# Kernel tuning notes

Hardware: AMD Instinct MI355X
Metric: run time of the kernel (lower is better)

## Reference

```python
import jax, jax.numpy as jnp
import numpy as np

NUM_OBJS = 180   # len(vocab['node'])
NUM_PREDS = 180  # len(vocab['edge'])
D = 128          # embedding_dim == gconv_dim
H = 512          # gconv_hidden_dim
L = 5            # gconv_num_layers (1 GraphTripleConv + 4 in GraphTripleConvNet; identical shapes)
G = 64           # number of graphs in the batch
O = 5000         # total nodes
T = 20000        # total triples (edges)
SC = 0.02        # param init scale


def setup_inputs() -> dict:
    key = jax.random.key(0)
    ks = jax.random.split(key, 18)
    objs = jax.random.randint(ks[0], (O,), 0, NUM_OBJS + 1)
    s = jax.random.randint(ks[1], (T,), 0, O)
    o = jax.random.randint(ks[2], (T,), 0, O)
    p = jax.random.randint(ks[3], (T,), 0, NUM_PREDS)
    triples = jnp.stack([s, p, o], axis=1)
    obj_to_img = jnp.sort(jax.random.randint(ks[4], (O,), 0, G))
    f32 = jnp.float32
    return {
        'objs': objs,
        'triples': triples,
        'obj_to_img': obj_to_img,
        'obj_emb': jax.random.normal(ks[5], (NUM_OBJS + 1, D), f32) * SC,
        'pred_emb': jax.random.normal(ks[6], (NUM_PREDS, D), f32) * SC,
        # net1: [3D -> H -> 2H + D], stacked over L layers
        'n1w1': jax.random.normal(ks[7], (L, 3 * D, H), f32) * SC,
        'n1b1': jnp.zeros((L, H), f32),
        'n1w2': jax.random.normal(ks[8], (L, H, 2 * H + D), f32) * SC,
        'n1b2': jnp.zeros((L, 2 * H + D), f32),
        # net2: [H -> H -> D], stacked over L layers
        'n2w1': jax.random.normal(ks[9], (L, H, H), f32) * SC,
        'n2b1': jnp.zeros((L, H), f32),
        'n2w2': jax.random.normal(ks[10], (L, H, D), f32) * SC,
        'n2b2': jnp.zeros((L, D), f32),
        # AttentionModule: per-graph attention pooling over node vectors
        'att_w': jax.random.normal(ks[11], (D,), f32) * SC,
        'att_b': jnp.zeros((), f32),
    }


def _mlp2(x, w1, b1, w2, b2):
    # build_mlp with final_nonlinearity=True -> Linear,ReLU,Linear,ReLU
    return jax.nn.relu(jax.nn.relu(x @ w1 + b1) @ w2 + b2)


def _triple_conv(ov, pv, s, o, n1w1, n1b1, n1w2, n1b2, n2w1, n2b1, n2w2, n2b2):
    n_obj = ov.shape[0]
    t = jnp.concatenate([ov[s], pv, ov[o]], axis=1)          # [T, 3D]
    new_t = _mlp2(t, n1w1, n1b1, n1w2, n1b2)                 # [T, 2H+D]
    new_s = new_t[:, :H]
    new_p = new_t[:, H:H + D]
    new_o = new_t[:, H + D:]
    pooled = jnp.zeros((n_obj, H), new_t.dtype).at[s].add(new_s).at[o].add(new_o)
    counts = jnp.zeros((n_obj,), new_t.dtype).at[s].add(1.0).at[o].add(1.0)
    pooled = pooled / jnp.clip(counts, 1.0)[:, None]         # pooling='avg'
    new_ov = _mlp2(pooled, n2w1, n2b1, n2w2, n2b2)           # [O, D]
    return new_ov, new_p


def reference(objs, triples, obj_to_img, obj_emb, pred_emb,
              n1w1, n1b1, n1w2, n1b2, n2w1, n2b1, n2w2, n2b2, att_w, att_b):
    s, p, o = triples[:, 0], triples[:, 1], triples[:, 2]
    ov = obj_emb[objs]     # [O, D]
    pv = pred_emb[p]       # [T, D]
    for l in range(L):
        ov, pv = _triple_conv(ov, pv, s, o,
                              n1w1[l], n1b1[l], n1w2[l], n1b2[l],
                              n2w1[l], n2b1[l], n2w2[l], n2b2[l])
    # AttentionModule: segment softmax attention pooling per graph, broadcast back
    scores = ov @ att_w + att_b                               # [O]
    m = jax.ops.segment_max(scores, obj_to_img, num_segments=G)
    e = jnp.exp(scores - m[obj_to_img])
    z = jax.ops.segment_sum(e, obj_to_img, num_segments=G)
    w = e / z[obj_to_img]
    g = jax.ops.segment_sum(w[:, None] * ov, obj_to_img, num_segments=G)  # [G, D]
    graph_vecs = g[obj_to_img]                                # [O, D]
    return jnp.concatenate([ov, graph_vecs], axis=1)          # [O, 2D]
```

## Files before the change

kernel.cpp:

```cpp
#include <hip/hip_runtime.h>
#include <math.h>

#define O_N 5000
#define T_N 20000
#define D_ 128
#define H_ 512
#define L_ 5
#define G_ 64
#define NT_ 1152
#define NPRED 180

typedef unsigned short ushort_t;
typedef __attribute__((ext_vector_type(8))) __bf16 bf16x8;
typedef __attribute__((ext_vector_type(4))) float f32x4;

__device__ inline float bf2f(ushort_t u) {
    union { unsigned u32; float f; } cv; cv.u32 = ((unsigned)u) << 16; return cv.f;
}
__device__ inline ushort_t f2bf(float f) {
    union { float f; unsigned u; } cv; cv.f = f;
    unsigned x = cv.u;
    unsigned r = x + 0x7FFFu + ((x >> 16) & 1u);
    return (ushort_t)(r >> 16);
}

__device__ inline void gload16(const void* g, void* l) {
    __builtin_amdgcn_global_load_lds(
        (const __attribute__((address_space(1))) unsigned int*)g,
        (__attribute__((address_space(3))) unsigned int*)l,
        16, 0, 0);
}

template<int GATHER, int WRITE_F32>
__global__ __launch_bounds__(256)
void mfma_gemm(const ushort_t* __restrict__ A,
               const ushort_t* __restrict__ Bt,
               const float* __restrict__ bias,
               ushort_t* __restrict__ Cb,
               float* __restrict__ Cf,
               int M, int N, int K, int ldc, int ntiles,
               const int* __restrict__ triples,
               const ushort_t* __restrict__ ovb,
               const ushort_t* __restrict__ P, int pstride, int pmap)
{
    __shared__ __align__(16) ushort_t smem[16384];

    const int tid  = threadIdx.x;
    const int lane = tid & 63;
    const int wid  = tid >> 6;
    const int wm   = wid & 1;
    const int wn   = wid >> 1;

    const int nwg = gridDim.x;
    const int q = nwg >> 3, r = nwg & 7;
    const int xcd = blockIdx.x & 7, i8 = blockIdx.x >> 3;
    const int lid = (xcd < r ? xcd * (q + 1) : r * (q + 1) + (xcd - r) * q) + i8;
    const int bm = (lid / ntiles) * 128;
    const int bn = (lid % ntiles) * 128;

    const int u0 = wid * 64 + lane;
    const int u1 = u0 + 256;
    const int r0 = u0 >> 2;
    const int r1 = u1 >> 2;
    const int ks0 = (((u0 & 3) ^ ((r0 >> 1) & 3)) << 3);
    const int ks1 = (((u1 & 3) ^ ((r1 >> 1) & 3)) << 3);

    const int ga0 = min(bm + r0, M - 1);
    const int ga1 = min(bm + r1, M - 1);
    int s0 = 0, o0 = 0, p0 = 0, s1 = 0, o1 = 0, p1 = 0;
    if (GATHER) {
        s0 = triples[ga0 * 3];  p0 = pmap ? triples[ga0 * 3 + 1] : ga0;  o0 = triples[ga0 * 3 + 2];
        s1 = triples[ga1 * 3];  p1 = pmap ? triples[ga1 * 3 + 1] : ga1;  o1 = triples[ga1 * 3 + 2];
    }
    const int gb0 = bn + r0;
    const int gb1 = bn + r1;

    int offA[4], offB[4];
    #pragma unroll
    for (int i = 0; i < 4; ++i) {
        int ra = wm * 64 + i * 16 + (lane & 15);
        offA[i] = (ra * 4 + ((lane >> 4) ^ ((ra >> 1) & 3))) << 3;
        int rb = wn * 64 + i * 16 + (lane & 15);
        offB[i] = (rb * 4 + ((lane >> 4) ^ ((rb >> 1) & 3))) << 3;
    }

    auto stage = [&](int k0, int buf) {
        ushort_t* Ab = smem + buf * 4096;
        ushort_t* Bb = smem + 8192 + buf * 4096;
        const ushort_t *gA0p, *gA1p;
        if (GATHER) {
            int k = k0 + ks0;
            gA0p = (k < 128) ? (ovb + (size_t)s0 * D_ + k)
                 : (k < 256) ? (P + (size_t)p0 * pstride + (k - 128))
                             : (ovb + (size_t)o0 * D_ + (k - 256));
            k = k0 + ks1;
            gA1p = (k < 128) ? (ovb + (size_t)s1 * D_ + k)
                 : (k < 256) ? (P + (size_t)p1 * pstride + (k - 128))
                             : (ovb + (size_t)o1 * D_ + (k - 256));
        } else {
            gA0p = A + (size_t)ga0 * K + k0 + ks0;
            gA1p = A + (size_t)ga1 * K + k0 + ks1;
        }
        gload16(gA0p, Ab + wid * 512);
        gload16(gA1p, Ab + 2048 + wid * 512);
        gload16(Bt + (size_t)gb0 * K + k0 + ks0, Bb + wid * 512);
        gload16(Bt + (size_t)gb1 * K + k0 + ks1, Bb + 2048 + wid * 512);
    };

    f32x4 acc[4][4] = {};

    const int nt = K >> 5;
    stage(0, 0);
    stage(32, 1);

    int cur = 0;
    for (int t = 0; t < nt - 1; ++t) {
        asm volatile("s_waitcnt vmcnt(4)" ::: "memory");
        __builtin_amdgcn_s_barrier();
        __builtin_amdgcn_sched_barrier(0);
        const ushort_t* Ar = smem + cur * 4096;
        const ushort_t* Br = smem + 8192 + cur * 4096;
        bf16x8 av[4], bv[4];
        #pragma unroll
        for (int i = 0; i < 4; ++i) av[i] = *(const bf16x8*)(Ar + offA[i]);
        #pragma unroll
        for (int i = 0; i < 4; ++i) bv[i] = *(const bf16x8*)(Br + offB[i]);
        asm volatile("s_waitcnt lgkmcnt(0)" ::: "memory");
        __builtin_amdgcn_sched_barrier(0);
        __builtin_amdgcn_s_barrier();
        if (t + 2 < nt) stage((t + 2) << 5, cur);
        #pragma unroll
        for (int mi = 0; mi < 4; ++mi)
            #pragma unroll
            for (int ni = 0; ni < 4; ++ni)
                acc[mi][ni] = __builtin_amdgcn_mfma_f32_16x16x32_bf16(
                    av[mi], bv[ni], acc[mi][ni], 0, 0, 0);
        cur ^= 1;
    }
    {
        asm volatile("s_waitcnt vmcnt(0)" ::: "memory");
        __builtin_amdgcn_s_barrier();
        __builtin_amdgcn_sched_barrier(0);
        const ushort_t* Ar = smem + cur * 4096;
        const ushort_t* Br = smem + 8192 + cur * 4096;
        bf16x8 av[4], bv[4];
        #pragma unroll
        for (int i = 0; i < 4; ++i) av[i] = *(const bf16x8*)(Ar + offA[i]);
        #pragma unroll
        for (int i = 0; i < 4; ++i) bv[i] = *(const bf16x8*)(Br + offB[i]);
        #pragma unroll
        for (int mi = 0; mi < 4; ++mi)
            #pragma unroll
            for (int ni = 0; ni < 4; ++ni)
                acc[mi][ni] = __builtin_amdgcn_mfma_f32_16x16x32_bf16(
                    av[mi], bv[ni], acc[mi][ni], 0, 0, 0);
    }
    __syncthreads();

    if (WRITE_F32) {
        #pragma unroll
        for (int ni = 0; ni < 4; ++ni) {
            int col = bn + wn * 64 + ni * 16 + (lane & 15);
            float bz = bias[col];
            #pragma unroll
            for (int mi = 0; mi < 4; ++mi) {
                int rowb = bm + wm * 64 + mi * 16 + ((lane >> 4) << 2);
                #pragma unroll
                for (int rr = 0; rr < 4; ++rr) {
                    int row = rowb + rr;
                    if (row < M) {
                        float v = fmaxf(acc[mi][ni][rr] + bz, 0.0f);
                        Cb[(size_t)row * ldc + col] = f2bf(v);
                        Cf[(size_t)row * ldc + col] = v;
                    }
                }
            }
        }
    } else {
        ushort_t* cst = smem + wid * 4096;
        #pragma unroll
        for (int ni = 0; ni < 4; ++ni) {
            int col = ni * 16 + (lane & 15);
            float bz = bias[bn + wn * 64 + col];
            #pragma unroll
            for (int mi = 0; mi < 4; ++mi) {
                int rowb = mi * 16 + ((lane >> 4) << 2);
                #pragma unroll
                for (int rr = 0; rr < 4; ++rr) {
                    float v = fmaxf(acc[mi][ni][rr] + bz, 0.0f);
                    cst[(rowb + rr) * 64 + col] = f2bf(v);
                }
            }
        }
        #pragma unroll
        for (int pp = 0; pp < 8; ++pp) {
            int wrow = pp * 8 + (lane >> 3);
            int grow = bm + wm * 64 + wrow;
            if (grow < M) {
                float4 v = *(const float4*)(cst + wrow * 64 + (lane & 7) * 8);
                *(float4*)(&Cb[(size_t)grow * ldc + bn + wn * 64 + (lane & 7) * 8]) = v;
            }
        }
    }
}

__global__ __launch_bounds__(256)
void precompute_kernel(const float* __restrict__ n1w1, const float* __restrict__ n1w2,
                       const float* __restrict__ n2w1, const float* __restrict__ n2w2,
                       ushort_t* __restrict__ w1t, ushort_t* __restrict__ w2t,
                       ushort_t* __restrict__ w3t, ushort_t* __restrict__ w4t,
                       const int* __restrict__ objs, const float* __restrict__ obj_emb,
                       const float* __restrict__ pred_emb,
                       ushort_t* __restrict__ ovb, ushort_t* __restrict__ predb,
                       int* __restrict__ cnt)
{
    int b = blockIdx.x;
    if (b < 5440) {
        int l = b / 1088, r = b % 1088;
        const float* src; ushort_t* dst; int K, N, n0, k0;
        if (r < 192)       { src = n1w1; dst = w1t; K = 384; N = 512;  n0 = (r % 16) * 32; k0 = (r / 16) * 32; }
        else if (r < 768)  { r -= 192;  src = n1w2; dst = w2t; K = 512; N = 1152; n0 = (r % 36) * 32; k0 = (r / 36) * 32; }
        else if (r < 1024) { r -= 768;  src = n2w1; dst = w3t; K = 512; N = 512;  n0 = (r % 16) * 32; k0 = (r / 16) * 32; }
        else               { r -= 1024; src = n2w2; dst = w4t; K = 512; N = 128;  n0 = (r % 4) * 32;  k0 = (r / 4) * 32; }
        __shared__ float t[32][33];
        const float* s = src + (size_t)l * K * N;
        ushort_t*    d = dst + (size_t)l * N * K;
        int rr = threadIdx.x >> 5, c = threadIdx.x & 31;
        #pragma unroll
        for (int j = 0; j < 4; ++j)
            t[rr + j * 8][c] = s[(size_t)(k0 + rr + j * 8) * N + n0 + c];
        __syncthreads();
        #pragma unroll
        for (int j = 0; j < 4; ++j)
            d[(size_t)(n0 + rr + j * 8) * K + k0 + c] = f2bf(t[c][rr + j * 8]);
    } else if (b < 8030) {
        int i = (b - 5440) * 256 + threadIdx.x;
        if (i < O_N * D_) ovb[i] = f2bf(obj_emb[(size_t)objs[i >> 7] * D_ + (i & 127)]);
        int j = i - O_N * D_;
        if (j >= 0 && j < NPRED * D_) predb[j] = f2bf(pred_emb[j]);
    } else {
        int i = (b - 8030) * 256 + threadIdx.x;
        if (i < O_N) cnt[i] = 0;
    }
}

__global__ void hist_kernel(const int* __restrict__ triples, int* __restrict__ cnt)
{
    int t = blockIdx.x * blockDim.x + threadIdx.x;
    if (t < T_N) {
        atomicAdd(&cnt[triples[t * 3]], 1);
        atomicAdd(&cnt[triples[t * 3 + 2]], 1);
    }
}

__global__ void scan_kernel(const int* __restrict__ cnt, int* __restrict__ off,
                            int* __restrict__ cursor)
{
    __shared__ int buf[256];
    __shared__ int base;
    int tid = threadIdx.x;
    if (tid == 0) base = 0;
    __syncthreads();
    for (int ch = 0; ch < O_N; ch += 256) {
        int v = (ch + tid < O_N) ? cnt[ch + tid] : 0;
        buf[tid] = v;
        __syncthreads();
        for (int s = 1; s < 256; s <<= 1) {
            int tmp = (tid >= s) ? buf[tid - s] : 0;
            __syncthreads();
            buf[tid] += tmp;
            __syncthreads();
        }
        int excl = base + buf[tid] - v;
        if (ch + tid < O_N) { off[ch + tid] = excl; cursor[ch + tid] = excl; }
        __syncthreads();
        if (tid == 0) base += buf[255];
        __syncthreads();
    }
    if (tid == 0) off[O_N] = base;
}

__global__ void fill_kernel(const int* __restrict__ triples, int* __restrict__ cursor,
                            int* __restrict__ entries)
{
    int t = blockIdx.x * blockDim.x + threadIdx.x;
    if (t < T_N) {
        int s = triples[t * 3], o = triples[t * 3 + 2];
        entries[atomicAdd(&cursor[s], 1)] = t * 2;
        entries[atomicAdd(&cursor[o], 1)] = t * 2 + 1;
    }
}

__global__ void pooled_kernel(const ushort_t* __restrict__ newt,
                              const int* __restrict__ entries,
                              const int* __restrict__ off,
                              ushort_t* __restrict__ pooled)
{
    int i = blockIdx.x, tid = threadIdx.x;
    int st = off[i], en = off[i + 1];
    float a0 = 0.f, a1 = 0.f, a2 = 0.f, a3 = 0.f;
    for (int e = st; e < en; ++e) {
        int ent = entries[e];
        const ushort_t* row = newt + (size_t)(ent >> 1) * NT_ + (ent & 1) * 640 + tid * 4;
        ushort4 v = *(const ushort4*)row;
        a0 += bf2f(v.x); a1 += bf2f(v.y); a2 += bf2f(v.z); a3 += bf2f(v.w);
    }
    int c = en - st; if (c < 1) c = 1;
    float sc = 1.0f / (float)c;
    ushort4 outv;
    outv.x = f2bf(a0 * sc); outv.y = f2bf(a1 * sc);
    outv.z = f2bf(a2 * sc); outv.w = f2bf(a3 * sc);
    *(ushort4*)(pooled + (size_t)i * H_ + tid * 4) = outv;
}

__global__ void scores_kernel(const float* __restrict__ ov,
                              const float* __restrict__ att_w,
                              const float* __restrict__ att_b,
                              float* __restrict__ scores)
{
    int gidx = blockIdx.x * blockDim.x + threadIdx.x;
    int obj = gidx >> 6;
    int lane = threadIdx.x & 63;
    if (obj >= O_N) return;
    const float* r = ov + (size_t)obj * D_;
    float v = r[lane] * att_w[lane] + r[lane + 64] * att_w[lane + 64];
    #pragma unroll
    for (int off = 32; off; off >>= 1) v += __shfl_down(v, off);
    if (lane == 0) scores[obj] = v + att_b[0];
}

__global__ __launch_bounds__(256)
void seg_gvec_kernel(const float* __restrict__ scores, const float* __restrict__ ovf,
                     const int* __restrict__ obj_to_img, float* __restrict__ gvec)
{
    __shared__ float red[256];
    __shared__ float sm, sz;
    int g = blockIdx.x, tid = threadIdx.x;
    int lo = 0, hi = O_N;
    while (lo < hi) { int mid = (lo + hi) >> 1; if (obj_to_img[mid] < g) lo = mid + 1; else hi = mid; }
    int st = lo;
    hi = O_N;
    while (lo < hi) { int mid = (lo + hi) >> 1; if (obj_to_img[mid] <= g) lo = mid + 1; else hi = mid; }
    int en = lo;

    float lm = -1e30f;
    for (int i = st + tid; i < en; i += 256) lm = fmaxf(lm, scores[i]);
    red[tid] = lm; __syncthreads();
    for (int s = 128; s; s >>= 1) { if (tid < s) red[tid] = fmaxf(red[tid], red[tid + s]); __syncthreads(); }
    if (tid == 0) sm = red[0];
    __syncthreads();
    float m = sm;

    float lz = 0.f;
    for (int i = st + tid; i < en; i += 256) lz += expf(scores[i] - m);
    red[tid] = lz; __syncthreads();
    for (int s = 128; s; s >>= 1) { if (tid < s) red[tid] += red[tid + s]; __syncthreads(); }
    if (tid == 0) sz = fmaxf(red[0], 1e-30f);
    __syncthreads();
    float invz = 1.0f / sz;

    int d = tid & 127, half = tid >> 7;
    float acc = 0.f;
    for (int i = st + half; i < en; i += 2)
        acc += expf(scores[i] - m) * ovf[(size_t)i * D_ + d];
    red[tid] = acc; __syncthreads();
    if (tid < 128) gvec[(size_t)g * D_ + tid] = (red[tid] + red[tid + 128]) * invz;
}

__global__ void output_kernel(const float* __restrict__ ov, const float* __restrict__ gvec,
                              const int* __restrict__ obj_to_img, float* __restrict__ out)
{
    int idx = blockIdx.x * blockDim.x + threadIdx.x;
    if (idx >= O_N * 256) return;
    int i = idx >> 8, d = idx & 255;
    out[idx] = (d < 128) ? ov[(size_t)i * D_ + d]
                         : gvec[obj_to_img[i] * D_ + (d - 128)];
}

extern "C" void kernel_launch(void* const* d_in, const int* in_sizes, int n_in,
                              void* d_out, int out_size, void* d_ws, size_t ws_size,
                              hipStream_t stream)
{
    const int*   objs       = (const int*)d_in[0];
    const int*   triples    = (const int*)d_in[1];
    const int*   obj_to_img = (const int*)d_in[2];
    const float* obj_emb    = (const float*)d_in[3];
    const float* pred_emb   = (const float*)d_in[4];
    const float* n1w1       = (const float*)d_in[5];
    const float* n1b1       = (const float*)d_in[6];
    const float* n1w2       = (const float*)d_in[7];
    const float* n1b2       = (const float*)d_in[8];
    const float* n2w1       = (const float*)d_in[9];
    const float* n2b1       = (const float*)d_in[10];
    const float* n2w2       = (const float*)d_in[11];
    const float* n2b2       = (const float*)d_in[12];
    const float* att_w      = (const float*)d_in[13];
    const float* att_b      = (const float*)d_in[14];
    float* out = (float*)d_out;

    char* p = (char*)d_ws;
    auto carve = [&](size_t bytes) -> char* {
        char* r = p; p += (bytes + 255) & ~(size_t)255; return r;
    };
    ushort_t* w1t     = (ushort_t*)carve((size_t)L_ * 512 * 384 * 2);
    ushort_t* w2t     = (ushort_t*)carve((size_t)L_ * 1152 * 512 * 2);
    ushort_t* w3t     = (ushort_t*)carve((size_t)L_ * 512 * 512 * 2);
    ushort_t* w4t     = (ushort_t*)carve((size_t)L_ * 128 * 512 * 2);
    ushort_t* ovbA    = (ushort_t*)carve((size_t)O_N * D_ * 2);
    ushort_t* ovbB    = (ushort_t*)carve((size_t)O_N * D_ * 2);
    ushort_t* predb   = (ushort_t*)carve((size_t)NPRED * D_ * 2);
    ushort_t* hiddenb = (ushort_t*)carve((size_t)T_N * H_ * 2);
    ushort_t* newtb   = (ushort_t*)carve((size_t)T_N * NT_ * 2);
    ushort_t* pooledb = (ushort_t*)carve((size_t)O_N * H_ * 2);
    float*    ovf     = (float*)carve((size_t)O_N * D_ * 4);
    float*    scores  = (float*)carve((size_t)O_N * 4);
    float*    gvec    = (float*)carve((size_t)G_ * D_ * 4);
    int*      cnt     = (int*)carve((size_t)O_N * 4);
    int*      off     = (int*)carve((size_t)(O_N + 1) * 4);
    int*      cursor  = (int*)carve((size_t)O_N * 4);
    int*      entries = (int*)carve((size_t)2 * T_N * 4);

    precompute_kernel<<<8050, 256, 0, stream>>>(
        n1w1, n1w2, n2w1, n2w2, w1t, w2t, w3t, w4t,
        objs, obj_emb, pred_emb, ovbA, predb, cnt);
    hist_kernel<<<(T_N + 255) / 256, 256, 0, stream>>>(triples, cnt);
    scan_kernel<<<1, 256, 0, stream>>>(cnt, off, cursor);
    fill_kernel<<<(T_N + 255) / 256, 256, 0, stream>>>(triples, cursor, entries);

    ushort_t* ovcur = ovbA;
    ushort_t* ovnxt = ovbB;

    for (int l = 0; l < L_; ++l) {
        const ushort_t* Pl = (l == 0) ? predb : (newtb + H_);
        int pstr = (l == 0) ? D_ : NT_;
        int pmap = (l == 0) ? 1 : 0;

        mfma_gemm<1, 0><<<157 * 4, 256, 0, stream>>>(
            nullptr, w1t + (size_t)l * 512 * 384, n1b1 + (size_t)l * H_,
            hiddenb, nullptr, T_N, 512, 384, H_, 4,
            triples, ovcur, Pl, pstr, pmap);

        mfma_gemm<0, 0><<<157 * 9, 256, 0, stream>>>(
            hiddenb, w2t + (size_t)l * 1152 * 512, n1b2 + (size_t)l * NT_,
            newtb, nullptr, T_N, NT_, 512, NT_, 9,
            nullptr, nullptr, nullptr, 0, 0);

        pooled_kernel<<<O_N, 128, 0, stream>>>(newtb, entries, off, pooledb);

        mfma_gemm<0, 0><<<40 * 4, 256, 0, stream>>>(
            pooledb, w3t + (size_t)l * 512 * 512, n2b1 + (size_t)l * H_,
            hiddenb, nullptr, O_N, 512, 512, H_, 4,
            nullptr, nullptr, nullptr, 0, 0);

        if (l < L_ - 1) {
            mfma_gemm<0, 0><<<40 * 1, 256, 0, stream>>>(
                hiddenb, w4t + (size_t)l * 128 * 512, n2b2 + (size_t)l * D_,
                ovnxt, nullptr, O_N, 128, 512, D_, 1,
                nullptr, nullptr, nullptr, 0, 0);
        } else {
            mfma_gemm<0, 1><<<40 * 1, 256, 0, stream>>>(
                hiddenb, w4t + (size_t)l * 128 * 512, n2b2 + (size_t)l * D_,
                ovnxt, ovf, O_N, 128, 512, D_, 1,
                nullptr, nullptr, nullptr, 0, 0);
        }

        ushort_t* tmp = ovcur; ovcur = ovnxt; ovnxt = tmp;
    }

    scores_kernel<<<(O_N * 64 + 255) / 256, 256, 0, stream>>>(ovf, att_w, att_b, scores);
    seg_gvec_kernel<<<G_, 256, 0, stream>>>(scores, ovf, obj_to_img, gvec);
    output_kernel<<<(O_N * 256 + 255) / 256, 256, 0, stream>>>(ovf, gvec, obj_to_img, out);
}
```

Baseline: 559.4 us.

## Triple-buffer GEMM LDS stages, drop second barrier, raise MFMA priority

The MFMA GEMM moves from a two-buffer to a three-buffer LDS ring. The next-next tile load is now issued right after the first barrier, which removes the second per-iteration barrier and the wait on LDS reads before it. The separate tail iteration is folded into the main loop, and s_setprio is raised around the MFMA block. The f32-output epilogue also stops writing the bf16 copy, which saves global stores but is only safe if nothing later reads Cb. LDS per block grows from 32 KB to 48 KB, which may lower occupancy.

Result: no change. 565.3 us (+1.1%).

```diff
diff --git a/kernel.cpp b/kernel.cpp
--- a/kernel.cpp
+++ b/kernel.cpp
@@ -43,7 +43,7 @@
                const ushort_t* __restrict__ ovb,
                const ushort_t* __restrict__ P, int pstride, int pmap)
 {
-    __shared__ __align__(16) ushort_t smem[16384];
+    __shared__ __align__(16) ushort_t smem[24576];
 
     const int tid  = threadIdx.x;
     const int lane = tid & 63;
@@ -86,7 +86,7 @@
 
     auto stage = [&](int k0, int buf) {
         ushort_t* Ab = smem + buf * 4096;
-        ushort_t* Bb = smem + 8192 + buf * 4096;
+        ushort_t* Bb = smem + 12288 + buf * 4096;
         const ushort_t *gA0p, *gA1p;
         if (GATHER) {
             int k = k0 + ks0;
@@ -113,47 +113,35 @@
     stage(0, 0);
     stage(32, 1);
 
-    int cur = 0;
-    for (int t = 0; t < nt - 1; ++t) {
-        asm volatile("s_waitcnt vmcnt(4)" ::: "memory");
+    int rb = 0;
+    for (int t = 0; t < nt; ++t) {
+        if (t < nt - 1) {
+            asm volatile("s_waitcnt vmcnt(4)" ::: "memory");
+        } else {
+            asm volatile("s_waitcnt vmcnt(0)" ::: "memory");
+        }
         __builtin_amdgcn_s_barrier();
         __builtin_amdgcn_sched_barrier(0);
-        const ushort_t* Ar = smem + cur * 4096;
-        const ushort_t* Br = smem + 8192 + cur * 4096;
+        if (t + 2 < nt) {
+            int sb = rb + 2; if (sb >= 3) sb -= 3;
+            stage((t + 2) << 5, sb);
+        }
+        const ushort_t* Ar = smem + rb * 4096;
+        const ushort_t* Br = smem + 12288 + rb * 4096;
         bf16x8 av[4], bv[4];
         #pragma unroll
         for (int i = 0; i < 4; ++i) av[i] = *(const bf16x8*)(Ar + offA[i]);
         #pragma unroll
         for (int i = 0; i < 4; ++i) bv[i] = *(const bf16x8*)(Br + offB[i]);
-        asm volatile("s_waitcnt lgkmcnt(0)" ::: "memory");
-        __builtin_amdgcn_sched_barrier(0);
-        __builtin_amdgcn_s_barrier();
-        if (t + 2 < nt) stage((t + 2) << 5, cur);
+        __builtin_amdgcn_s_setprio(1);
         #pragma unroll
         for (int mi = 0; mi < 4; ++mi)
             #pragma unroll
             for (int ni = 0; ni < 4; ++ni)
                 acc[mi][ni] = __builtin_amdgcn_mfma_f32_16x16x32_bf16(
                     av[mi], bv[ni], acc[mi][ni], 0, 0, 0);
-        cur ^= 1;
-    }
-    {
-        asm volatile("s_waitcnt vmcnt(0)" ::: "memory");
-        __builtin_amdgcn_s_barrier();
-        __builtin_amdgcn_sched_barrier(0);
-        const ushort_t* Ar = smem + cur * 4096;
-        const ushort_t* Br = smem + 8192 + cur * 4096;
-        bf16x8 av[4], bv[4];
-        #pragma unroll
-        for (int i = 0; i < 4; ++i) av[i] = *(const bf16x8*)(Ar + offA[i]);
-        #pragma unroll
-        for (int i = 0; i < 4; ++i) bv[i] = *(const bf16x8*)(Br + offB[i]);
-        #pragma unroll
-        for (int mi = 0; mi < 4; ++mi)
-            #pragma unroll
-            for (int ni = 0; ni < 4; ++ni)
-                acc[mi][ni] = __builtin_amdgcn_mfma_f32_16x16x32_bf16(
-                    av[mi], bv[ni], acc[mi][ni], 0, 0, 0);
+        __builtin_amdgcn_s_setprio(0);
+        rb = (rb == 2) ? 0 : rb + 1;
     }
     __syncthreads();
 
@@ -170,7 +158,6 @@
                     int row = rowb + rr;
                     if (row < M) {
                         float v = fmaxf(acc[mi][ni][rr] + bz, 0.0f);
-                        Cb[(size_t)row * ldc + col] = f2bf(v);
                         Cf[(size_t)row * ldc + col] = v;
                     }
                 }
```
